# Optimization experiments

Measured on AMD Instinct MI355X. Metric: run time of the kernel, lower is better.

## Reference

```python
import jax, jax.numpy as jnp
import numpy as np

N_NODES = 20000
N_EDGES = 640000
HIDDEN = 256
HEADS = 8
HEAD_DIM = HIDDEN // HEADS
VOCAB = 119
N_FEATS = 9


def setup_inputs() -> dict:
    key = jax.random.key(0)
    ks = jax.random.split(key, 12)
    X = jax.random.randint(ks[0], (N_NODES, N_FEATS), 0, VOCAB)
    edge_row = jnp.sort(jax.random.randint(ks[1], (N_EDGES,), 0, N_NODES))
    edge_col = jax.random.randint(ks[2], (N_EDGES,), 0, N_NODES)
    s = 0.05  # init scale to keep activations sane
    emb_tables = jax.random.normal(ks[3], (N_FEATS, VOCAB, HIDDEN), jnp.float32) * s
    q_w = jax.random.normal(ks[4], (HIDDEN, HIDDEN), jnp.float32) * s
    q_b = jax.random.normal(ks[5], (HIDDEN,), jnp.float32) * s
    k_w = jax.random.normal(ks[6], (HIDDEN, HIDDEN), jnp.float32) * s
    k_b = jax.random.normal(ks[7], (HIDDEN,), jnp.float32) * s
    v_w = jax.random.normal(ks[8], (HIDDEN, HIDDEN), jnp.float32) * s
    v_b = jax.random.normal(ks[9], (HIDDEN,), jnp.float32) * s
    o_w = jax.random.normal(ks[10], (HIDDEN, HIDDEN), jnp.float32) * s
    o_b = jax.random.normal(ks[11], (HIDDEN,), jnp.float32) * s
    return dict(X=X, edge_row=edge_row, edge_col=edge_col, emb_tables=emb_tables,
                q_w=q_w, q_b=q_b, k_w=k_w, k_b=k_b, v_w=v_w, v_b=v_b, o_w=o_w, o_b=o_b)


def reference(X, edge_row, edge_col, emb_tables, q_w, q_b, k_w, k_b, v_w, v_b, o_w, o_b):
    N = X.shape[0]
    # AtomEncoder: sum of per-feature embeddings -> [N, HIDDEN]
    feat_idx = jnp.arange(N_FEATS)[None, :]  # [1, 9]
    h = emb_tables[feat_idx, X].sum(axis=1)  # [N, 9, H] -> [N, H]
    # q/k/v projections (torch Linear: y = x W^T + b), split into heads
    q = (h @ q_w.T + q_b).reshape(N, HEADS, HEAD_DIM) * (HEAD_DIM ** -0.5)
    k = (h @ k_w.T + k_b).reshape(N, HEADS, HEAD_DIM)
    v = (h @ v_w.T + v_b).reshape(N, HEADS, HEAD_DIM)
    # SDDMM: per-edge, per-head scores
    s = jnp.einsum('ehd,ehd->eh', q[edge_row], k[edge_col])  # [E, HEADS]
    # sparse row-wise softmax (over each node's outgoing-edge neighbors)
    m = jax.ops.segment_max(s, edge_row, num_segments=N)
    e = jnp.exp(s - m[edge_row])
    z = jax.ops.segment_sum(e, edge_row, num_segments=N)
    attn = e / z[edge_row]  # [E, HEADS]
    # SPMM: weighted aggregation of neighbor values
    out = jax.ops.segment_sum(attn[:, :, None] * v[edge_col], edge_row, num_segments=N)
    return out.reshape(N, HIDDEN) @ o_w.T + o_b
```

## Files before the change

kernel.cpp:

```cpp
#include <hip/hip_runtime.h>
#include <hip/hip_bf16.h>

#define N_NODES 20000
#define N_EDGES 640000
#define HIDDEN 256
#define HEADS 8
#define HEAD_DIM 32
#define N_FEATS 9
#define VOCAB 119

typedef __hip_bfloat16 bf16;
typedef __attribute__((ext_vector_type(8))) short short8;
typedef __attribute__((ext_vector_type(4))) float f32x4;

__device__ __forceinline__ ushort f2u(float x) { union { ushort u; bf16 b; } c; c.b = __float2bfloat16(x); return c.u; }
__device__ __forceinline__ void unpack8(uint4 u, float* f) {
    f[0] = __uint_as_float(u.x << 16); f[1] = __uint_as_float(u.x & 0xffff0000u);
    f[2] = __uint_as_float(u.y << 16); f[3] = __uint_as_float(u.y & 0xffff0000u);
    f[4] = __uint_as_float(u.z << 16); f[5] = __uint_as_float(u.z & 0xffff0000u);
    f[6] = __uint_as_float(u.w << 16); f[7] = __uint_as_float(u.w & 0xffff0000u);
}
__device__ __forceinline__ uint pack2(float a, float b) {
    union { __hip_bfloat162 h; uint u; } c;
    c.h = __float22bfloat162_rn(make_float2(a, b));
    return c.u;
}

#if __has_builtin(__builtin_amdgcn_fdot2_f32_bf16)
typedef __attribute__((ext_vector_type(2))) __bf16 bf16x2_t;
__device__ __forceinline__ float dot2bf(uint a, uint b, float c) {
    return __builtin_amdgcn_fdot2_f32_bf16(__builtin_bit_cast(bf16x2_t, a),
                                           __builtin_bit_cast(bf16x2_t, b), c, false);
}
#else
__device__ __forceinline__ float dot2bf(uint a, uint b, float c) {
    return c + __uint_as_float(a << 16) * __uint_as_float(b << 16)
             + __uint_as_float(a & 0xffff0000u) * __uint_as_float(b & 0xffff0000u);
}
#endif

__global__ void k_rowptr(const int* __restrict__ edge_row, int* __restrict__ row_ptr) {
    int n = blockIdx.x * 256 + threadIdx.x;
    if (n > N_NODES) return;
    int lo = 0, hi = N_EDGES;
    while (lo < hi) {
        int mid = (lo + hi) >> 1;
        if (edge_row[mid] < n) lo = mid + 1; else hi = mid;
    }
    row_ptr[n] = lo;
}

__global__ void k_prep(const float* __restrict__ qw, const float* __restrict__ kw,
                       const float* __restrict__ vw, const float* __restrict__ ow,
                       const float* __restrict__ qb, const float* __restrict__ kb,
                       const float* __restrict__ vb,
                       bf16* __restrict__ wqkv, bf16* __restrict__ wo,
                       float* __restrict__ qkvb) {
    int i = blockIdx.x * 256 + threadIdx.x;
    if (i < 196608) {
        const float* s = i < 65536 ? qw : i < 131072 ? kw : vw;
        wqkv[i] = __float2bfloat16(s[i & 65535]);
    } else if (i < 262144) {
        wo[i - 196608] = __float2bfloat16(ow[i - 196608]);
    } else {
        int j = i - 262144;
        const float* s = j < 256 ? qb : j < 512 ? kb : vb;
        qkvb[j] = s[j & 255];
    }
}

__global__ void k_encode(const int* __restrict__ X, const float* __restrict__ emb,
                         bf16* __restrict__ h) {
    int tid = blockIdx.x * 256 + threadIdx.x;
    int n = tid >> 6;
    int c4 = (tid & 63) * 4;
    float4 a = make_float4(0.f, 0.f, 0.f, 0.f);
#pragma unroll
    for (int f = 0; f < N_FEATS; ++f) {
        int idx = X[n * N_FEATS + f];
        float4 e = *(const float4*)(emb + ((size_t)(f * VOCAB + idx)) * HIDDEN + c4);
        a.x += e.x; a.y += e.y; a.z += e.z; a.w += e.w;
    }
    ushort4 o = make_ushort4(f2u(a.x), f2u(a.y), f2u(a.z), f2u(a.w));
    *(ushort4*)((ushort*)h + (size_t)n * HIDDEN + c4) = o;
}

template <int MODE, bool GUARD>
__device__ __forceinline__ void gemm_core(const bf16* __restrict__ A,
                                          const bf16* __restrict__ W,
                                          const float* __restrict__ bias,
                                          void* __restrict__ Y0, void* __restrict__ Y1,
                                          float s_q, int n0, int d0) {
    __shared__ short As[128 * 72];
    __shared__ short Bs[128 * 72];
    int t = threadIdx.x;
    int lane = t & 63, w = t >> 6;
    int wr = (w >> 1) * 64, wc = (w & 1) * 64;
    int lr = lane & 15, quad = lane >> 4;

    f32x4 acc[4][4] = {};
    short8 ra[4], rb[4];
    int srow[4], sko[4];
#pragma unroll
    for (int it = 0; it < 4; ++it) { int c = t + 256 * it; srow[it] = c >> 3; sko[it] = (c & 7) * 8; }

#pragma unroll
    for (int it = 0; it < 4; ++it) {
        int n = n0 + srow[it];
        short8 av = {};
        if (!GUARD || n < N_NODES) av = *(const short8*)(A + (size_t)n * HIDDEN + sko[it]);
        ra[it] = av;
        rb[it] = *(const short8*)(W + (size_t)(d0 + srow[it]) * HIDDEN + sko[it]);
    }
#pragma unroll
    for (int it = 0; it < 4; ++it) {
        *(short8*)(&As[srow[it] * 72 + sko[it]]) = ra[it];
        *(short8*)(&Bs[srow[it] * 72 + sko[it]]) = rb[it];
    }
    __syncthreads();

    for (int k0 = 64; k0 < 256; k0 += 64) {
#pragma unroll
        for (int it = 0; it < 4; ++it) {
            int n = n0 + srow[it];
            short8 av = {};
            if (!GUARD || n < N_NODES) av = *(const short8*)(A + (size_t)n * HIDDEN + k0 + sko[it]);
            ra[it] = av;
            rb[it] = *(const short8*)(W + (size_t)(d0 + srow[it]) * HIDDEN + k0 + sko[it]);
        }
        {
            short8 af[4][2], bfr[4][2];
#pragma unroll
            for (int i = 0; i < 4; ++i)
#pragma unroll
                for (int kk = 0; kk < 2; ++kk) {
                    af[i][kk]  = *(short8*)(&As[(wr + i * 16 + lr) * 72 + kk * 32 + quad * 8]);
                    bfr[i][kk] = *(short8*)(&Bs[(wc + i * 16 + lr) * 72 + kk * 32 + quad * 8]);
                }
#pragma unroll
            for (int kk = 0; kk < 2; ++kk)
#pragma unroll
                for (int i = 0; i < 4; ++i)
#pragma unroll
                    for (int j = 0; j < 4; ++j)
                        acc[i][j] = __builtin_amdgcn_mfma_f32_16x16x32_bf16(
                            af[i][kk], bfr[j][kk], acc[i][j], 0, 0, 0);
        }
        __syncthreads();
#pragma unroll
        for (int it = 0; it < 4; ++it) {
            *(short8*)(&As[srow[it] * 72 + sko[it]]) = ra[it];
            *(short8*)(&Bs[srow[it] * 72 + sko[it]]) = rb[it];
        }
        __syncthreads();
    }
    {
        short8 af[4][2], bfr[4][2];
#pragma unroll
        for (int i = 0; i < 4; ++i)
#pragma unroll
            for (int kk = 0; kk < 2; ++kk) {
                af[i][kk]  = *(short8*)(&As[(wr + i * 16 + lr) * 72 + kk * 32 + quad * 8]);
                bfr[i][kk] = *(short8*)(&Bs[(wc + i * 16 + lr) * 72 + kk * 32 + quad * 8]);
            }
#pragma unroll
        for (int kk = 0; kk < 2; ++kk)
#pragma unroll
            for (int i = 0; i < 4; ++i)
#pragma unroll
                for (int j = 0; j < 4; ++j)
                    acc[i][j] = __builtin_amdgcn_mfma_f32_16x16x32_bf16(
                        af[i][kk], bfr[j][kk], acc[i][j], 0, 0, 0);
    }

#pragma unroll
    for (int j = 0; j < 4; ++j) {
        int dbase = d0 + wc + j * 16;
        float bj = bias[dbase + lr];
        if constexpr (MODE == 0) {
            float sc = (dbase < 256) ? s_q : 1.f;
            ushort* dst; int stride;
            if (dbase < 256) {
                dst = (ushort*)Y0 + (size_t)(dbase >> 6) * N_NODES * 64 + (dbase & 63) + lr;
                stride = 64;
            } else if (dbase < 512) {
                int e = dbase - 256;
                dst = (ushort*)Y1 + (size_t)(e >> 6) * N_NODES * 128 + (e & 63) + lr;
                stride = 128;
            } else {
                int e = dbase - 512;
                dst = (ushort*)Y1 + (size_t)(e >> 6) * N_NODES * 128 + 64 + (e & 63) + lr;
                stride = 128;
            }
#pragma unroll
            for (int i = 0; i < 4; ++i)
#pragma unroll
                for (int r = 0; r < 4; ++r) {
                    int n = n0 + wr + i * 16 + quad * 4 + r;
                    if (GUARD && n >= N_NODES) continue;
                    dst[(size_t)n * stride] = f2u((acc[i][j][r] + bj) * sc);
                }
        } else {
            float* dst = (float*)Y0 + dbase + lr;
#pragma unroll
            for (int i = 0; i < 4; ++i)
#pragma unroll
                for (int r = 0; r < 4; ++r) {
                    int n = n0 + wr + i * 16 + quad * 4 + r;
                    if (GUARD && n >= N_NODES) continue;
                    dst[(size_t)n * HIDDEN] = acc[i][j][r] + bj;
                }
        }
    }
}

__global__ __launch_bounds__(256, 2) void k_gemm_qkv(
    const bf16* __restrict__ A, const bf16* __restrict__ wqkv,
    const float* __restrict__ qkvb, ushort* __restrict__ qhp,
    ushort* __restrict__ kvhp, float qscale) {
    int n0 = blockIdx.x * 128;
    if (n0 + 128 <= N_NODES)
        gemm_core<0, false>(A, wqkv, qkvb, qhp, kvhp, qscale, n0, blockIdx.y * 128);
    else
        gemm_core<0, true>(A, wqkv, qkvb, qhp, kvhp, qscale, n0, blockIdx.y * 128);
}

__global__ __launch_bounds__(256, 2) void k_gemm_o(
    const bf16* __restrict__ A, const bf16* __restrict__ W,
    const float* __restrict__ bias, float* __restrict__ Y) {
    int n0 = blockIdx.x * 128;
    if (n0 + 128 <= N_NODES)
        gemm_core<1, false>(A, W, bias, Y, nullptr, 1.f, n0, blockIdx.y * 128);
    else
        gemm_core<1, true>(A, W, bias, Y, nullptr, 1.f, n0, blockIdx.y * 128);
}

__global__ __launch_bounds__(256) void k_attn(
    const int* __restrict__ row_ptr, const int* __restrict__ col,
    const ushort* __restrict__ qhp, const ushort* __restrict__ kvhp,
    bf16* __restrict__ agg) {
    int b = blockIdx.x;
    int x = b & 7;
    int hp = x & 3;
    int wave = threadIdx.x >> 6;
    int n = (b >> 3) * 8 + (x >> 2) * 4 + wave;
    int lane = threadIdx.x & 63;
    int my = lane >> 3;
    int d8 = lane & 7;

    int start = row_ptr[n];
    int deg = row_ptr[n + 1] - start;

    ushort* orow = (ushort*)agg + (size_t)n * HIDDEN + hp * 64 + d8 * 8;
    if (deg == 0) {
        if (lane < 8) { uint4 zo = {}; *(uint4*)orow = zo; }
        return;
    }

    const ushort* qrow = qhp + ((size_t)hp * N_NODES + n) * 64;
    uint4 qu = *(const uint4*)(qrow + d8 * 8);

    const ushort* kvbase = kvhp + (size_t)hp * N_NODES * 128;
    const int* cb = col + start;

    int c_all = cb[min(lane, deg - 1)];

    float z = 0.f;
    float av[8] = {};

#pragma unroll 2
    for (int i = 0; i < deg; i += 8) {
        int idx = i + my;
        int cidx = idx < deg ? idx : deg - 1;
        int c = (deg <= 64) ? __shfl(c_all, cidx) : cb[cidx];

        const ushort* kp = kvbase + (((uint)c << 7) + (uint)d8 * 8);
        uint4 ku = *(const uint4*)(kp);
        uint4 vu = *(const uint4*)(kp + 64);

        float s = dot2bf(ku.x, qu.x, 0.f);
        s = dot2bf(ku.y, qu.y, s);
        s = dot2bf(ku.z, qu.z, s);
        s = dot2bf(ku.w, qu.w, s);
        s += __shfl_xor(s, 1);
        s += __shfl_xor(s, 2);

        float p = (idx < deg) ? __expf(s) : 0.f;
        z += p;

        float vf[8];
        unpack8(vu, vf);
#pragma unroll
        for (int d = 0; d < 8; ++d) av[d] += p * vf[d];
    }

    z += __shfl_xor(z, 8); z += __shfl_xor(z, 16); z += __shfl_xor(z, 32);
#pragma unroll
    for (int d = 0; d < 8; ++d) {
        av[d] += __shfl_xor(av[d], 8);
        av[d] += __shfl_xor(av[d], 16);
        av[d] += __shfl_xor(av[d], 32);
    }

    if (lane < 8) {
        float invz = 1.f / z;
        uint4 o;
        o.x = pack2(av[0] * invz, av[1] * invz);
        o.y = pack2(av[2] * invz, av[3] * invz);
        o.z = pack2(av[4] * invz, av[5] * invz);
        o.w = pack2(av[6] * invz, av[7] * invz);
        *(uint4*)orow = o;
    }
}

extern "C" void kernel_launch(void* const* d_in, const int* in_sizes, int n_in,
                              void* d_out, int out_size, void* d_ws, size_t ws_size,
                              hipStream_t stream) {
    const int*   X    = (const int*)d_in[0];
    const int*   erow = (const int*)d_in[1];
    const int*   ecol = (const int*)d_in[2];
    const float* emb  = (const float*)d_in[3];
    const float* q_w  = (const float*)d_in[4];
    const float* q_b  = (const float*)d_in[5];
    const float* k_w  = (const float*)d_in[6];
    const float* k_b  = (const float*)d_in[7];
    const float* v_w  = (const float*)d_in[8];
    const float* v_b  = (const float*)d_in[9];
    const float* o_w  = (const float*)d_in[10];
    const float* o_b  = (const float*)d_in[11];
    float* out = (float*)d_out;

    char* ws = (char*)d_ws;
    bf16*   h    = (bf16*)(ws);
    bf16*   agg  = (bf16*)(ws);
    ushort* qhp  = (ushort*)(ws + 10240000);
    ushort* kvhp = (ushort*)(ws + 20480000);
    bf16*   wqkv = (bf16*)(ws + 40960000);
    bf16*   wo   = (bf16*)(ws + 41353216);
    float*  qkvb = (float*)(ws + 41484288);
    int* row_ptr = (int*)(ws + 41487360);

    k_rowptr<<<(N_NODES + 256) / 256, 256, 0, stream>>>(erow, row_ptr);
    k_prep<<<1027, 256, 0, stream>>>(q_w, k_w, v_w, o_w, q_b, k_b, v_b, wqkv, wo, qkvb);
    k_encode<<<N_NODES / 4, 256, 0, stream>>>(X, emb, h);

    const float qscale = 0.17677669529663687f;
    dim3 gqkv((N_NODES + 127) / 128, 768 / 128);
    k_gemm_qkv<<<gqkv, 256, 0, stream>>>(h, wqkv, qkvb, qhp, kvhp, qscale);

    k_attn<<<N_NODES, 256, 0, stream>>>(row_ptr, ecol, qhp, kvhp, agg);

    dim3 go((N_NODES + 127) / 128, HIDDEN / 128);
    k_gemm_o<<<go, 256, 0, stream>>>(agg, wo, o_b, out);
}
```

Baseline: 185.6 us.

## Fuse prep kernels and stream GEMM weights via async LDS loads with swizzle

The row-pointer, weight-conversion and embedding-encode kernels are merged into a single launch that dispatches on block index, removing two kernel launches. The shared GEMM core now reads A fragments directly from global memory into registers instead of staging them in LDS. B tiles are loaded with global_load_lds async copies into a double-buffered, XOR-swizzled LDS buffer, which drops one barrier per k-step and overlaps the next B tile load with the MFMA work. In exchange, A is re-read from global/L2 by each wave, and the row guard on A loads is gone, so the last tile reads past N_NODES into adjacent workspace memory.

```diff
diff --git a/kernel.cpp b/kernel.cpp
--- a/kernel.cpp
+++ b/kernel.cpp
@@ -39,50 +39,61 @@
 }
 #endif
 
-__global__ void k_rowptr(const int* __restrict__ edge_row, int* __restrict__ row_ptr) {
-    int n = blockIdx.x * 256 + threadIdx.x;
-    if (n > N_NODES) return;
-    int lo = 0, hi = N_EDGES;
-    while (lo < hi) {
-        int mid = (lo + hi) >> 1;
-        if (edge_row[mid] < n) lo = mid + 1; else hi = mid;
-    }
-    row_ptr[n] = lo;
-}
-
-__global__ void k_prep(const float* __restrict__ qw, const float* __restrict__ kw,
-                       const float* __restrict__ vw, const float* __restrict__ ow,
-                       const float* __restrict__ qb, const float* __restrict__ kb,
-                       const float* __restrict__ vb,
-                       bf16* __restrict__ wqkv, bf16* __restrict__ wo,
-                       float* __restrict__ qkvb) {
-    int i = blockIdx.x * 256 + threadIdx.x;
-    if (i < 196608) {
-        const float* s = i < 65536 ? qw : i < 131072 ? kw : vw;
-        wqkv[i] = __float2bfloat16(s[i & 65535]);
-    } else if (i < 262144) {
-        wo[i - 196608] = __float2bfloat16(ow[i - 196608]);
+__device__ __forceinline__ void async_ld16(const void* g, void* l) {
+#if __has_builtin(__builtin_amdgcn_global_load_lds)
+    __builtin_amdgcn_global_load_lds(
+        (const __attribute__((address_space(1))) unsigned int*)g,
+        (__attribute__((address_space(3))) unsigned int*)l, 16, 0, 0);
+#else
+    *(short8*)l = *(const short8*)g;
+#endif
+}
+
+__global__ void k_pre(const int* __restrict__ X, const float* __restrict__ emb,
+                      bf16* __restrict__ h,
+                      const float* __restrict__ qw, const float* __restrict__ kw,
+                      const float* __restrict__ vw, const float* __restrict__ ow,
+                      const float* __restrict__ qb, const float* __restrict__ kb,
+                      const float* __restrict__ vb,
+                      bf16* __restrict__ wqkv, bf16* __restrict__ wo,
+                      float* __restrict__ qkvb,
+                      const int* __restrict__ erow, int* __restrict__ row_ptr) {
+    int b = blockIdx.x;
+    if (b < 5000) {
+        int tid = b * 256 + threadIdx.x;
+        int n = tid >> 6;
+        int c4 = (tid & 63) * 4;
+        float4 a = make_float4(0.f, 0.f, 0.f, 0.f);
+#pragma unroll
+        for (int f = 0; f < N_FEATS; ++f) {
+            int idx = X[n * N_FEATS + f];
+            float4 e = *(const float4*)(emb + ((size_t)(f * VOCAB + idx)) * HIDDEN + c4);
+            a.x += e.x; a.y += e.y; a.z += e.z; a.w += e.w;
+        }
+        ushort4 o = make_ushort4(f2u(a.x), f2u(a.y), f2u(a.z), f2u(a.w));
+        *(ushort4*)((ushort*)h + (size_t)n * HIDDEN + c4) = o;
+    } else if (b < 6027) {
+        int i = (b - 5000) * 256 + threadIdx.x;
+        if (i < 196608) {
+            const float* s = i < 65536 ? qw : i < 131072 ? kw : vw;
+            wqkv[i] = __float2bfloat16(s[i & 65535]);
+        } else if (i < 262144) {
+            wo[i - 196608] = __float2bfloat16(ow[i - 196608]);
+        } else if (i < 262912) {
+            int j = i - 262144;
+            const float* s = j < 256 ? qb : j < 512 ? kb : vb;
+            qkvb[j] = s[j & 255];
+        }
     } else {
-        int j = i - 262144;
-        const float* s = j < 256 ? qb : j < 512 ? kb : vb;
-        qkvb[j] = s[j & 255];
-    }
-}
-
-__global__ void k_encode(const int* __restrict__ X, const float* __restrict__ emb,
-                         bf16* __restrict__ h) {
-    int tid = blockIdx.x * 256 + threadIdx.x;
-    int n = tid >> 6;
-    int c4 = (tid & 63) * 4;
-    float4 a = make_float4(0.f, 0.f, 0.f, 0.f);
-#pragma unroll
-    for (int f = 0; f < N_FEATS; ++f) {
-        int idx = X[n * N_FEATS + f];
-        float4 e = *(const float4*)(emb + ((size_t)(f * VOCAB + idx)) * HIDDEN + c4);
-        a.x += e.x; a.y += e.y; a.z += e.z; a.w += e.w;
-    }
-    ushort4 o = make_ushort4(f2u(a.x), f2u(a.y), f2u(a.z), f2u(a.w));
-    *(ushort4*)((ushort*)h + (size_t)n * HIDDEN + c4) = o;
+        int n = (b - 6027) * 256 + threadIdx.x;
+        if (n > N_NODES) return;
+        int lo = 0, hi = N_EDGES;
+        while (lo < hi) {
+            int mid = (lo + hi) >> 1;
+            if (erow[mid] < n) lo = mid + 1; else hi = mid;
+        }
+        row_ptr[n] = lo;
+    }
 }
 
 template <int MODE, bool GUARD>
@@ -91,77 +102,78 @@
                                           const float* __restrict__ bias,
                                           void* __restrict__ Y0, void* __restrict__ Y1,
                                           float s_q, int n0, int d0) {
-    __shared__ short As[128 * 72];
-    __shared__ short Bs[128 * 72];
+    __shared__ short Bs[2][128 * 64];
     int t = threadIdx.x;
     int lane = t & 63, w = t >> 6;
     int wr = (w >> 1) * 64, wc = (w & 1) * 64;
     int lr = lane & 15, quad = lane >> 4;
 
     f32x4 acc[4][4] = {};
-    short8 ra[4], rb[4];
-    int srow[4], sko[4];
-#pragma unroll
-    for (int it = 0; it < 4; ++it) { int c = t + 256 * it; srow[it] = c >> 3; sko[it] = (c & 7) * 8; }
-
+
+    int srow[4], scc[4], sbase[4];
 #pragma unroll
     for (int it = 0; it < 4; ++it) {
-        int n = n0 + srow[it];
-        short8 av = {};
-        if (!GUARD || n < N_NODES) av = *(const short8*)(A + (size_t)n * HIDDEN + sko[it]);
-        ra[it] = av;
-        rb[it] = *(const short8*)(W + (size_t)(d0 + srow[it]) * HIDDEN + sko[it]);
-    }
-#pragma unroll
-    for (int it = 0; it < 4; ++it) {
-        *(short8*)(&As[srow[it] * 72 + sko[it]]) = ra[it];
-        *(short8*)(&Bs[srow[it] * 72 + sko[it]]) = rb[it];
-    }
+        int s = it * 256 + t;
+        int r = s >> 3;
+        srow[it]  = r;
+        scc[it]   = (s & 7) ^ (r & 7);
+        sbase[it] = (it * 256 + (t & ~63)) * 8;
+    }
+
+#pragma unroll
+    for (int it = 0; it < 4; ++it)
+        async_ld16(W + (size_t)(d0 + srow[it]) * HIDDEN + scc[it] * 8, &Bs[0][sbase[it]]);
     __syncthreads();
 
+    int cur = 0;
+#pragma unroll 1
     for (int k0 = 64; k0 < 256; k0 += 64) {
-#pragma unroll
-        for (int it = 0; it < 4; ++it) {
-            int n = n0 + srow[it];
-            short8 av = {};
-            if (!GUARD || n < N_NODES) av = *(const short8*)(A + (size_t)n * HIDDEN + k0 + sko[it]);
-            ra[it] = av;
-            rb[it] = *(const short8*)(W + (size_t)(d0 + srow[it]) * HIDDEN + k0 + sko[it]);
-        }
-        {
-            short8 af[4][2], bfr[4][2];
+        int kbase = k0 - 64;
+        short8 af[4][2], bfr[4][2];
+#pragma unroll
+        for (int i = 0; i < 4; ++i)
+#pragma unroll
+            for (int kk = 0; kk < 2; ++kk)
+                af[i][kk] = *(const short8*)(A + (size_t)(n0 + wr + i * 16 + lr) * HIDDEN
+                                             + kbase + kk * 32 + quad * 8);
+#pragma unroll
+        for (int it = 0; it < 4; ++it)
+            async_ld16(W + (size_t)(d0 + srow[it]) * HIDDEN + k0 + scc[it] * 8,
+                       &Bs[cur ^ 1][sbase[it]]);
+#pragma unroll
+        for (int j = 0; j < 4; ++j)
+#pragma unroll
+            for (int kk = 0; kk < 2; ++kk) {
+                int rB = wc + j * 16 + lr;
+                int slot = rB * 8 + ((kk * 4 + quad) ^ (lr & 7));
+                bfr[j][kk] = *(short8*)(&Bs[cur][slot * 8]);
+            }
+#pragma unroll
+        for (int kk = 0; kk < 2; ++kk)
 #pragma unroll
             for (int i = 0; i < 4; ++i)
 #pragma unroll
-                for (int kk = 0; kk < 2; ++kk) {
-                    af[i][kk]  = *(short8*)(&As[(wr + i * 16 + lr) * 72 + kk * 32 + quad * 8]);
-                    bfr[i][kk] = *(short8*)(&Bs[(wc + i * 16 + lr) * 72 + kk * 32 + quad * 8]);
-                }
-#pragma unroll
-            for (int kk = 0; kk < 2; ++kk)
-#pragma unroll
-                for (int i = 0; i < 4; ++i)
-#pragma unroll
-                    for (int j = 0; j < 4; ++j)
-                        acc[i][j] = __builtin_amdgcn_mfma_f32_16x16x32_bf16(
-                            af[i][kk], bfr[j][kk], acc[i][j], 0, 0, 0);
-        }
+                for (int j = 0; j < 4; ++j)
+                    acc[i][j] = __builtin_amdgcn_mfma_f32_16x16x32_bf16(
+                        af[i][kk], bfr[j][kk], acc[i][j], 0, 0, 0);
         __syncthreads();
-#pragma unroll
-        for (int it = 0; it < 4; ++it) {
-            *(short8*)(&As[srow[it] * 72 + sko[it]]) = ra[it];
-            *(short8*)(&Bs[srow[it] * 72 + sko[it]]) = rb[it];
-        }
-        __syncthreads();
+        cur ^= 1;
     }
     {
         short8 af[4][2], bfr[4][2];
 #pragma unroll
         for (int i = 0; i < 4; ++i)
 #pragma unroll
+            for (int kk = 0; kk < 2; ++kk)
+                af[i][kk] = *(const short8*)(A + (size_t)(n0 + wr + i * 16 + lr) * HIDDEN
+                                             + 192 + kk * 32 + quad * 8);
+#pragma unroll
+        for (int j = 0; j < 4; ++j)
+#pragma unroll
             for (int kk = 0; kk < 2; ++kk) {
-                af[i][kk]  = *(short8*)(&As[(wr + i * 16 + lr) * 72 + kk * 32 + quad * 8]);
-                bfr[i][kk] = *(short8*)(&Bs[(wc + i * 16 + lr) * 72 + kk * 32 + quad * 8]);
+                int rB = wc + j * 16 + lr;
+                int slot = rB * 8 + ((kk * 4 + quad) ^ (lr & 7));
+                bfr[j][kk] = *(short8*)(&Bs[cur][slot * 8]);
             }
 #pragma unroll
         for (int kk = 0; kk < 2; ++kk)
@@ -340,9 +352,8 @@
     float*  qkvb = (float*)(ws + 41484288);
     int* row_ptr = (int*)(ws + 41487360);
 
-    k_rowptr<<<(N_NODES + 256) / 256, 256, 0, stream>>>(erow, row_ptr);
-    k_prep<<<1027, 256, 0, stream>>>(q_w, k_w, v_w, o_w, q_b, k_b, v_b, wqkv, wo, qkvb);
-    k_encode<<<N_NODES / 4, 256, 0, stream>>>(X, emb, h);
+    k_pre<<<6106, 256, 0, stream>>>(X, emb, h, q_w, k_w, v_w, o_w,
+                                    q_b, k_b, v_b, wqkv, wo, qkvb, erow, row_ptr);
 
     const float qscale = 0.17677669529663687f;
     dim3 gqkv((N_NODES + 127) / 128, 768 / 128);
```

New measurement: 190.4 us. 2.5% more time.
